# Performance work log

Measured on AMD Instinct MI355X. Metric: run time of the kernel, lower is better.

The kernel has to match this reference:

```python
import jax, jax.numpy as jnp
import numpy as np

B, L, C_IN, H, MID = 8192, 256, 6, 32, 128  # batch, knots, input_channels, hidden_channels, MLP width


def setup_inputs() -> dict:
    key = jax.random.key(0)
    ks = jax.random.split(key, 8)
    cshape = (B, L - 1, C_IN)
    times = jnp.arange(L, dtype=jnp.float32)
    # spline coefficients (a, b, two_c, three_d); small scale keeps the CDE stable
    coeff_a = jax.random.normal(ks[0], cshape, dtype=jnp.float32) * 0.05
    coeff_b = jax.random.normal(ks[1], cshape, dtype=jnp.float32) * 0.05
    coeff_c = jax.random.normal(ks[2], cshape, dtype=jnp.float32) * 0.05
    coeff_d = jax.random.normal(ks[3], cshape, dtype=jnp.float32) * 0.05
    # CDEFunc params: Linear(H->128), Linear(128->H*C_IN); readout Linear(H->C_IN)
    W1 = jax.random.normal(ks[4], (H, MID), dtype=jnp.float32) / np.float32(np.sqrt(H))
    b1 = jnp.zeros((MID,), dtype=jnp.float32)
    W2 = jax.random.normal(ks[5], (MID, H * C_IN), dtype=jnp.float32) / np.float32(np.sqrt(MID))
    b2 = jnp.zeros((H * C_IN,), dtype=jnp.float32)
    Wl = jax.random.normal(ks[6], (H, C_IN), dtype=jnp.float32) / np.float32(np.sqrt(H))
    bl = jnp.zeros((C_IN,), dtype=jnp.float32)
    return dict(times=times, coeff_a=coeff_a, coeff_b=coeff_b, coeff_c=coeff_c,
                coeff_d=coeff_d, W1=W1, b1=b1, W2=W2, b2=b2, Wl=Wl, bl=bl)


def reference(times, coeff_a, coeff_b, coeff_c, coeff_d, W1, b1, W2, b2, Wl, bl):
    # dz/dt = f(z) @ dX/dt, integrated t[0] -> t[-1] (RK4, one step per spline interval).
    def vf(z, dx):
        h = jnp.tanh(z @ W1 + b1)                       # (B, 128)
        g = (h @ W2 + b2).reshape(z.shape[0], H, C_IN)  # (B, H, C_IN)
        return jnp.einsum('bhi,bi->bh', g, dx)          # (B, H)

    dts = times[1:] - times[:-1]                        # (L-1,)
    bs = jnp.moveaxis(coeff_b, 1, 0)                    # (L-1, B, C)
    cs = jnp.moveaxis(coeff_c, 1, 0)
    ds = jnp.moveaxis(coeff_d, 1, 0)
    z0 = jnp.zeros((coeff_b.shape[0], H), dtype=times.dtype)

    def step(z, xs):
        dt, bi, ci, di = xs
        dX = lambda f: bi + ci * f + di * (f * f)       # spline derivative b + 2c*f + 3d*f^2
        k1 = vf(z, dX(0.0))
        k2 = vf(z + 0.5 * dt * k1, dX(0.5 * dt))
        k3 = vf(z + 0.5 * dt * k2, dX(0.5 * dt))
        k4 = vf(z + dt * k3, dX(dt))
        return z + (dt / 6.0) * (k1 + 2.0 * k2 + 2.0 * k3 + k4), None

    zT, _ = jax.lax.scan(step, z0, (dts, bs, cs, ds))
    return zT @ Wl + bl                                 # (B, C_IN)
```

## Files before the change

### kernel.cpp

```cpp
#include <hip/hip_runtime.h>


typedef _Float16 half8 __attribute__((ext_vector_type(8)));
typedef _Float16 half4 __attribute__((ext_vector_type(4)));
typedef float floatx4 __attribute__((ext_vector_type(4)));

constexpr int B_TOT  = 8192;
constexpr int L      = 256;
constexpr int CIN    = 6;
constexpr int H      = 32;
constexpr int MID    = 128;
constexpr int NSTEPS = L - 1;
constexpr int NB     = 16;
constexpr int WG     = 256;

constexpr int HP  = 152;
constexpr int ZSP = 72;
constexpr int GIS = 33;
constexpr int GBS = 199;
constexpr int ZP  = 33;

constexpr float RSC  = 2048.f;
constexpr float IRSC = 1.f / 2048.f;

__global__ __launch_bounds__(WG, 1)
void cde_hybrid_kernel(const float* __restrict__ times,
                       const float* __restrict__ coeff_b,
                       const float* __restrict__ coeff_c,
                       const float* __restrict__ coeff_d,
                       const float* __restrict__ W1g,
                       const float* __restrict__ b1g,
                       const float* __restrict__ W2g,
                       const float* __restrict__ b2g,
                       const float* __restrict__ Wlg,
                       const float* __restrict__ blg,
                       float* __restrict__ out)
{
    __shared__ __align__(16) _Float16 sHh[NB][HP], sHl[NB][HP];
    __shared__ float sGf[NB * GBS + 4];
    __shared__ __align__(16) _Float16 sZh[NB][ZSP], sZl[NB][ZSP];
    __shared__ float sDx[3][NB][8];
    __shared__ float sFin[NB][ZP];

    const int tid  = threadIdx.x;
    const int lane = tid & 63;
    const int wave = tid >> 6;
    const int l15  = lane & 15;
    const int q    = lane >> 4;
    const int b0   = blockIdx.x * NB;

    half8 w2h[3][4], w2l[3][4];
    float b2v[3];
    int   gofs[3];
    #pragma unroll
    for (int f = 0; f < 3; ++f) {
        const int n = (wave * 3 + f) * 16 + l15;
        b2v[f]  = b2g[n];
        gofs[f] = (n % 6) * GIS + (n / 6);
        #pragma unroll
        for (int ks = 0; ks < 4; ++ks) {
            #pragma unroll
            for (int j = 0; j < 8; ++j) {
                const float w = W2g[(ks * 32 + q * 8 + j) * (H * CIN) + n];
                const _Float16 hh = (_Float16)w;
                w2h[f][ks][j] = hh;
                w2l[f][ks][j] = (_Float16)((w - (float)hh) * RSC);
            }
        }
    }

    half8 w1h[2], w1l[2];
    float b1v[2][4];
    #pragma unroll
    for (int f1 = 0; f1 < 2; ++f1) {
        const int mt = wave * 2 + f1;
        #pragma unroll
        for (int j = 0; j < 8; ++j) {
            const float w = W1g[(q * 8 + j) * MID + mt * 16 + l15];
            const _Float16 hh = (_Float16)w;
            w1h[f1][j] = hh;
            w1l[f1][j] = (_Float16)((w - (float)hh) * RSC);
        }
        #pragma unroll
        for (int r = 0; r < 4; ++r)
            b1v[f1][r] = b1g[mt * 16 + q * 4 + r];
    }

    float za[2] = {0.f, 0.f};
    float zb[2] = {0.f, 0.f};
    for (int i = tid; i < NB * ZSP; i += WG) {
        (&sZh[0][0])[i] = (_Float16)0.f; (&sZl[0][0])[i] = (_Float16)0.f;
    }
    __syncthreads();

    for (int t = 0; t < NSTEPS; ++t) {
        const float dt = times[t + 1] - times[t];
        if (tid < NB * CIN) {
            const int bb = tid / CIN, ii = tid - bb * CIN;
            const size_t off = ((size_t)(b0 + bb) * NSTEPS + t) * CIN + ii;
            const float vb = coeff_b[off], vc = coeff_c[off], vd = coeff_d[off];
            const float f1 = 0.5f * dt;
            sDx[0][bb][ii] = vb;
            sDx[1][bb][ii] = vb + vc * f1 + vd * f1 * f1;
            sDx[2][bb][ii] = vb + vc * dt + vd * dt * dt;
        }
        __syncthreads();

        #pragma unroll 1
        for (int s = 0; s < 4; ++s) {
            const half8 zh = *(const half8*)&sZh[l15][q * 8];
            const half8 zl = *(const half8*)&sZl[l15][q * 8];
            floatx4 ht[2], htr[2];
            #pragma unroll
            for (int f1 = 0; f1 < 2; ++f1) {
                ht[f1]  = floatx4{0.f, 0.f, 0.f, 0.f};
                htr[f1] = floatx4{0.f, 0.f, 0.f, 0.f};
            }
            #pragma unroll
            for (int f1 = 0; f1 < 2; ++f1) {
                ht[f1]  = __builtin_amdgcn_mfma_f32_16x16x32_f16(w1h[f1], zh, ht[f1],  0, 0, 0);
                htr[f1] = __builtin_amdgcn_mfma_f32_16x16x32_f16(w1l[f1], zh, htr[f1], 0, 0, 0);
                htr[f1] = __builtin_amdgcn_mfma_f32_16x16x32_f16(w1h[f1], zl, htr[f1], 0, 0, 0);
            }
            #pragma unroll
            for (int f1 = 0; f1 < 2; ++f1) {
                const int mt = wave * 2 + f1;
                half4 vh, vl;
                #pragma unroll
                for (int r = 0; r < 4; ++r) {
                    const float pre = ht[f1][r] + htr[f1][r] * IRSC + b1v[f1][r];
                    const float e = __expf(2.f * pre);
                    const float h = 1.f - 2.f / (e + 1.f);
                    const _Float16 hh = (_Float16)h;
                    vh[r] = hh;
                    vl[r] = (_Float16)((h - (float)hh) * RSC);
                }
                *(half4*)&sHh[l15][mt * 16 + q * 4] = vh;
                *(half4*)&sHl[l15][mt * 16 + q * 4] = vl;
            }
            __syncthreads();

            floatx4 g[3], gr[3];
            #pragma unroll
            for (int f = 0; f < 3; ++f) {
                g[f]  = floatx4{0.f, 0.f, 0.f, 0.f};
                gr[f] = floatx4{0.f, 0.f, 0.f, 0.f};
            }
            #pragma unroll
            for (int ks = 0; ks < 4; ++ks) {
                const half8 ah = *(const half8*)&sHh[l15][ks * 32 + q * 8];
                const half8 al = *(const half8*)&sHl[l15][ks * 32 + q * 8];
                #pragma unroll
                for (int f = 0; f < 3; ++f) {
                    g[f]  = __builtin_amdgcn_mfma_f32_16x16x32_f16(ah, w2h[f][ks], g[f],  0, 0, 0);
                    gr[f] = __builtin_amdgcn_mfma_f32_16x16x32_f16(al, w2h[f][ks], gr[f], 0, 0, 0);
                    gr[f] = __builtin_amdgcn_mfma_f32_16x16x32_f16(ah, w2l[f][ks], gr[f], 0, 0, 0);
                }
            }
            #pragma unroll
            for (int f = 0; f < 3; ++f) {
                #pragma unroll
                for (int r = 0; r < 4; ++r)
                    sGf[(q * 4 + r) * GBS + gofs[f]] = g[f][r] + gr[f][r] * IRSC + b2v[f];
            }
            __syncthreads();

            const int dsel = (s == 0) ? 0 : ((s == 3) ? 2 : 1);
            const float ws = (s == 0 || s == 3) ? dt * (1.f / 6.f) : dt * (1.f / 3.f);
            const int o  = tid & 31;
            const int bA = tid >> 5, bB = bA + 8;
            #pragma unroll
            for (int jj = 0; jj < 2; ++jj) {
                const int b = (jj == 0) ? bA : bB;
                float k = 0.f;
                #pragma unroll
                for (int i = 0; i < 6; ++i)
                    k += sGf[b * GBS + i * GIS + o] * sDx[dsel][b][i];
                const float zan = za[jj] + ws * k;
                za[jj] = zan;
                float zc;
                if (s < 3) {
                    zc = zb[jj] + ((s == 2) ? dt : 0.5f * dt) * k;
                } else {
                    zb[jj] = zan;
                    zc = zan;
                }
                const _Float16 zh0 = (_Float16)zc;
                sZh[b][o] = zh0;
                sZl[b][o] = (_Float16)((zc - (float)zh0) * RSC);
            }
            __syncthreads();
        }
    }

    {
        const int o = tid & 31, bA = tid >> 5;
        sFin[bA][o]     = zb[0];
        sFin[bA + 8][o] = zb[1];
    }
    __syncthreads();
    if (tid < NB * CIN) {
        const int bb = tid / CIN, c = tid - bb * CIN;
        float acc = blg[c];
        #pragma unroll
        for (int o = 0; o < H; ++o) acc += sFin[bb][o] * Wlg[o * CIN + c];
        out[(size_t)(b0 + bb) * CIN + c] = acc;
    }
}

extern "C" void kernel_launch(void* const* d_in, const int* in_sizes, int n_in,
                              void* d_out, int out_size, void* d_ws, size_t ws_size,
                              hipStream_t stream) {
    const float* times = (const float*)d_in[0];
    const float* cb = (const float*)d_in[2];
    const float* cc = (const float*)d_in[3];
    const float* cd = (const float*)d_in[4];
    const float* W1 = (const float*)d_in[5];
    const float* b1 = (const float*)d_in[6];
    const float* W2 = (const float*)d_in[7];
    const float* b2 = (const float*)d_in[8];
    const float* Wl = (const float*)d_in[9];
    const float* bl = (const float*)d_in[10];
    float* out = (float*)d_out;

    hipLaunchKernelGGL(cde_hybrid_kernel, dim3(B_TOT / NB), dim3(WG), 0, stream,
                       times, cb, cc, cd, W1, b1, W2, b2, Wl, bl, out);
}
```

Before: 2.295 ms.

## Keep z state in MFMA operand registers and prefetch spline coefficients

Each lane now computes the RK4 state update for exactly the 8 hidden entries it feeds as the B operand of the first MFMA (batch row l15, columns q*8..q*8+7). z therefore stays in registers as half8 hi/lo pairs, which drops the shared z buffers and one barrier per stage. The G layout in shared memory becomes a contiguous per-batch row read with float4 loads. Spline coefficients for the next step are loaded from global during stage 0 and written into a double-buffered dx array at stage 3, which removes the per-step barrier and global load latency. The cost is that every wave redundantly computes the whole state update, giving more registers per thread and duplicated arithmetic.

```diff
diff --git a/kernel.cpp b/kernel.cpp
--- a/kernel.cpp
+++ b/kernel.cpp
@@ -4,6 +4,7 @@
 typedef _Float16 half8 __attribute__((ext_vector_type(8)));
 typedef _Float16 half4 __attribute__((ext_vector_type(4)));
 typedef float floatx4 __attribute__((ext_vector_type(4)));
+typedef float floatx2 __attribute__((ext_vector_type(2)));
 
 constexpr int B_TOT  = 8192;
 constexpr int L      = 256;
@@ -15,9 +16,8 @@
 constexpr int WG     = 256;
 
 constexpr int HP  = 152;
-constexpr int ZSP = 72;
-constexpr int GIS = 33;
-constexpr int GBS = 199;
+constexpr int NST = 52;
+constexpr int DXS = 12;
 constexpr int ZP  = 33;
 
 constexpr float RSC  = 2048.f;
@@ -37,9 +37,8 @@
                        float* __restrict__ out)
 {
     __shared__ __align__(16) _Float16 sHh[NB][HP], sHl[NB][HP];
-    __shared__ float sGf[NB * GBS + 4];
-    __shared__ __align__(16) _Float16 sZh[NB][ZSP], sZl[NB][ZSP];
-    __shared__ float sDx[3][NB][8];
+    __shared__ __align__(16) float sGf[NB * NST];
+    __shared__ __align__(16) float sDx[2][3][NB][DXS];
     __shared__ float sFin[NB][ZP];
 
     const int tid  = threadIdx.x;
@@ -51,12 +50,10 @@
 
     half8 w2h[3][4], w2l[3][4];
     float b2v[3];
-    int   gofs[3];
     #pragma unroll
     for (int f = 0; f < 3; ++f) {
         const int n = (wave * 3 + f) * 16 + l15;
-        b2v[f]  = b2g[n];
-        gofs[f] = (n % 6) * GIS + (n / 6);
+        b2v[f] = b2g[n];
         #pragma unroll
         for (int ks = 0; ks < 4; ++ks) {
             #pragma unroll
@@ -86,30 +83,31 @@
             b1v[f1][r] = b1g[mt * 16 + q * 4 + r];
     }
 
-    float za[2] = {0.f, 0.f};
-    float zb[2] = {0.f, 0.f};
-    for (int i = tid; i < NB * ZSP; i += WG) {
-        (&sZh[0][0])[i] = (_Float16)0.f; (&sZl[0][0])[i] = (_Float16)0.f;
+    float za[8], zb[8];
+    half8 zh = {}, zl = {};
+    #pragma unroll
+    for (int oj = 0; oj < 8; ++oj) { za[oj] = 0.f; zb[oj] = 0.f; }
+
+    const bool dxo = tid < NB * CIN;
+    const int dxb = tid / CIN, dxi = tid - dxb * CIN;
+    if (dxo) {
+        const size_t off = ((size_t)(b0 + dxb) * NSTEPS + 0) * CIN + dxi;
+        const float vb = coeff_b[off], vc = coeff_c[off], vd = coeff_d[off];
+        const float dt0 = times[1] - times[0], f1 = 0.5f * dt0;
+        sDx[0][0][dxb][dxi] = vb;
+        sDx[0][1][dxb][dxi] = vb + vc * f1 + vd * f1 * f1;
+        sDx[0][2][dxb][dxi] = vb + vc * dt0 + vd * dt0 * dt0;
     }
     __syncthreads();
+
+    float pb = 0.f, pc = 0.f, pd = 0.f;
 
     for (int t = 0; t < NSTEPS; ++t) {
         const float dt = times[t + 1] - times[t];
-        if (tid < NB * CIN) {
-            const int bb = tid / CIN, ii = tid - bb * CIN;
-            const size_t off = ((size_t)(b0 + bb) * NSTEPS + t) * CIN + ii;
-            const float vb = coeff_b[off], vc = coeff_c[off], vd = coeff_d[off];
-            const float f1 = 0.5f * dt;
-            sDx[0][bb][ii] = vb;
-            sDx[1][bb][ii] = vb + vc * f1 + vd * f1 * f1;
-            sDx[2][bb][ii] = vb + vc * dt + vd * dt * dt;
-        }
-        __syncthreads();
+        const int cur = t & 1;
 
         #pragma unroll 1
         for (int s = 0; s < 4; ++s) {
-            const half8 zh = *(const half8*)&sZh[l15][q * 8];
-            const half8 zl = *(const half8*)&sZl[l15][q * 8];
             floatx4 ht[2], htr[2];
             #pragma unroll
             for (int f1 = 0; f1 < 2; ++f1) {
@@ -121,6 +119,10 @@
                 ht[f1]  = __builtin_amdgcn_mfma_f32_16x16x32_f16(w1h[f1], zh, ht[f1],  0, 0, 0);
                 htr[f1] = __builtin_amdgcn_mfma_f32_16x16x32_f16(w1l[f1], zh, htr[f1], 0, 0, 0);
                 htr[f1] = __builtin_amdgcn_mfma_f32_16x16x32_f16(w1h[f1], zl, htr[f1], 0, 0, 0);
+            }
+            if (s == 0 && dxo && t + 1 < NSTEPS) {
+                const size_t off = ((size_t)(b0 + dxb) * NSTEPS + (t + 1)) * CIN + dxi;
+                pb = coeff_b[off]; pc = coeff_c[off]; pd = coeff_d[off];
             }
             #pragma unroll
             for (int f1 = 0; f1 < 2; ++f1) {
@@ -138,6 +140,12 @@
                 *(half4*)&sHh[l15][mt * 16 + q * 4] = vh;
                 *(half4*)&sHl[l15][mt * 16 + q * 4] = vl;
             }
+            if (s == 3 && dxo && t + 1 < NSTEPS) {
+                const float dtn = times[t + 2] - times[t + 1], f1n = 0.5f * dtn;
+                sDx[cur ^ 1][0][dxb][dxi] = pb;
+                sDx[cur ^ 1][1][dxb][dxi] = pb + pc * f1n + pd * f1n * f1n;
+                sDx[cur ^ 1][2][dxb][dxi] = pb + pc * dtn + pd * dtn * dtn;
+            }
             __syncthreads();
 
             floatx4 g[3], gr[3];
@@ -159,44 +167,50 @@
             }
             #pragma unroll
             for (int f = 0; f < 3; ++f) {
+                const int n = (wave * 3 + f) * 16 + l15;
                 #pragma unroll
                 for (int r = 0; r < 4; ++r)
-                    sGf[(q * 4 + r) * GBS + gofs[f]] = g[f][r] + gr[f][r] * IRSC + b2v[f];
+                    sGf[(q * 4 + r) * NST + n] = g[f][r] + gr[f][r] * IRSC + b2v[f];
             }
             __syncthreads();
 
             const int dsel = (s == 0) ? 0 : ((s == 3) ? 2 : 1);
             const float ws = (s == 0 || s == 3) ? dt * (1.f / 6.f) : dt * (1.f / 3.f);
-            const int o  = tid & 31;
-            const int bA = tid >> 5, bB = bA + 8;
-            #pragma unroll
-            for (int jj = 0; jj < 2; ++jj) {
-                const int b = (jj == 0) ? bA : bB;
+            floatx4 gv[12];
+            #pragma unroll
+            for (int c = 0; c < 12; ++c)
+                gv[c] = *(const floatx4*)&sGf[l15 * NST + 48 * q + 4 * c];
+            const floatx4 d04 = *(const floatx4*)&sDx[cur][dsel][l15][0];
+            const floatx2 d02 = *(const floatx2*)&sDx[cur][dsel][l15][4];
+            const float dx6[6] = {d04[0], d04[1], d04[2], d04[3], d02[0], d02[1]};
+            #pragma unroll
+            for (int oj = 0; oj < 8; ++oj) {
                 float k = 0.f;
                 #pragma unroll
-                for (int i = 0; i < 6; ++i)
-                    k += sGf[b * GBS + i * GIS + o] * sDx[dsel][b][i];
-                const float zan = za[jj] + ws * k;
-                za[jj] = zan;
+                for (int i = 0; i < 6; ++i) {
+                    const int idx = 6 * oj + i;
+                    k += gv[idx >> 2][idx & 3] * dx6[i];
+                }
+                const float zan = za[oj] + ws * k;
+                za[oj] = zan;
                 float zc;
                 if (s < 3) {
-                    zc = zb[jj] + ((s == 2) ? dt : 0.5f * dt) * k;
+                    zc = zb[oj] + ((s == 2) ? dt : 0.5f * dt) * k;
                 } else {
-                    zb[jj] = zan;
+                    zb[oj] = zan;
                     zc = zan;
                 }
-                const _Float16 zh0 = (_Float16)zc;
-                sZh[b][o] = zh0;
-                sZl[b][o] = (_Float16)((zc - (float)zh0) * RSC);
-            }
-            __syncthreads();
+                const _Float16 h0 = (_Float16)zc;
+                zh[oj] = h0;
+                zl[oj] = (_Float16)((zc - (float)h0) * RSC);
+            }
         }
     }
 
-    {
-        const int o = tid & 31, bA = tid >> 5;
-        sFin[bA][o]     = zb[0];
-        sFin[bA + 8][o] = zb[1];
+    if (wave == 0) {
+        #pragma unroll
+        for (int oj = 0; oj < 8; ++oj)
+            sFin[l15][q * 8 + oj] = zb[oj];
     }
     __syncthreads();
     if (tid < NB * CIN) {
```

Result: slower. 3.225 ms (+40.5%).
